# Optimization experiments

Hardware: AMD Instinct MI355X
Metric: run time of the kernel (lower is better)

Reference implementation:

```python
import jax, jax.numpy as jnp
import numpy as np

N_NODES = 2048
N_FLUID = 400000
N_SOLID = 400000


def setup_inputs() -> dict:
    key = jax.random.key(0)
    k1, k2, k3 = jax.random.split(key, 3)
    nodes = jax.random.uniform(k1, (N_NODES, 3), dtype=jnp.float32)
    # sorted distinct node ids per tet: sort 4 draws from [0, N-4) then add offsets 0..3
    fe = jnp.sort(jax.random.randint(k2, (N_FLUID, 4), 0, N_NODES - 4), axis=1) + jnp.arange(4)
    se = jnp.sort(jax.random.randint(k3, (N_SOLID, 4), 0, N_NODES - 4), axis=1) + jnp.arange(4)
    return {
        "nodes": nodes,
        "fluid_elements": fe.astype(jnp.int32),
        "solid_elements": se.astype(jnp.int32),
        "E_mod": jnp.float32(2.1e11),
        "nu": jnp.float32(0.3),
        "rho_s": jnp.float32(7850.0),
    }


def _grads_and_volume(coords):
    """coords: [E,4,3] -> shape-fn gradients [E,4,3], volume [E]."""
    ones = jnp.ones(coords.shape[:-1] + (1,), coords.dtype)
    A = jnp.concatenate([ones, coords], axis=-1)
    A_inv = jnp.linalg.inv(A)
    grads = jnp.swapaxes(A_inv[..., 1:, :], -1, -2)        # [E,4,3]
    v0 = coords[:, 1] - coords[:, 0]
    v1 = coords[:, 2] - coords[:, 0]
    v2 = coords[:, 3] - coords[:, 0]
    vol = jnp.abs(jnp.linalg.det(jnp.stack([v0, v1, v2], axis=-1))) / 6.0  # [E]
    return grads, vol


def _fluid_element_matrices(coords):
    grads, vol = _grads_and_volume(coords)
    K_e = vol[:, None, None] * jnp.einsum("eik,ejk->eij", grads, grads)      # [E,4,4]
    m_template = (2.0 * jnp.eye(4, dtype=coords.dtype) + jnp.ones((4, 4), coords.dtype)) / 10.0
    M_e = vol[:, None, None] * m_template
    return K_e, M_e


def _elasticity_D(E_mod, nu):
    coeff = E_mod / ((1.0 + nu) * (1.0 - 2.0 * nu))
    top = nu * jnp.ones((3, 3), jnp.float32) + (1.0 - 2.0 * nu) * jnp.eye(3, dtype=jnp.float32)
    D = jnp.zeros((6, 6), jnp.float32)
    D = D.at[:3, :3].set(top)
    D = D.at[3:, 3:].set(((1.0 - 2.0 * nu) / 2.0) * jnp.eye(3, dtype=jnp.float32))
    return coeff * D


def _solid_element_matrices(coords, E_mod, nu, rho_s):
    grads, vol = _grads_and_volume(coords)                 # grads [E,4,3]
    bx, by, bz = grads[..., 0], grads[..., 1], grads[..., 2]   # each [E,4]
    z = jnp.zeros_like(bx)
    # per-node 6x3 strain-displacement block -> [E,4,6,3]
    block = jnp.stack([
        jnp.stack([bx, z, z], axis=-1),
        jnp.stack([z, by, z], axis=-1),
        jnp.stack([z, z, bz], axis=-1),
        jnp.stack([by, bx, z], axis=-1),
        jnp.stack([z, bz, by], axis=-1),
        jnp.stack([bz, z, bx], axis=-1),
    ], axis=-2)
    E = coords.shape[0]
    B = jnp.transpose(block, (0, 2, 1, 3)).reshape(E, 6, 12)  # [E,6,12]
    D = _elasticity_D(E_mod, nu)                              # [6,6]
    K_e = vol[:, None, None] * jnp.einsum("eai,ab,ebj->eij", B, D, B)  # [E,12,12]
    M_e = (rho_s * vol / 4.0)[:, None, None] * jnp.eye(12, dtype=coords.dtype)
    return K_e, M_e


def reference(nodes, fluid_elements, solid_elements, E_mod, nu, rho_s):
    n = nodes.shape[0]
    # ---- fluid: local matrices + scatter-add assembly into [N,N] ----
    cf = nodes[fluid_elements]                              # [Ef,4,3]
    Kf_e, Mf_e = _fluid_element_matrices(cf)
    rows = fluid_elements[:, :, None]                       # [Ef,4,1]
    cols = fluid_elements[:, None, :]                       # [Ef,1,4]
    K_f = jnp.zeros((n, n), jnp.float32).at[rows, cols].add(Kf_e)
    M_f = jnp.zeros((n, n), jnp.float32).at[rows, cols].add(Mf_e)
    # ---- solid: 3 dof/node, assembly into [3N,3N] ----
    cs = nodes[solid_elements]                              # [Es,4,3]
    Ks_e, Ms_e = _solid_element_matrices(cs, E_mod, nu, rho_s)
    dofs = (3 * solid_elements[:, :, None] + jnp.arange(3)).reshape(solid_elements.shape[0], 12)
    K_s = jnp.zeros((3 * n, 3 * n), jnp.float32).at[dofs[:, :, None], dofs[:, None, :]].add(Ks_e)
    M_s = jnp.zeros((3 * n, 3 * n), jnp.float32).at[dofs[:, :, None], dofs[:, None, :]].add(Ms_e)
    return (K_f, M_f, K_s, M_s)
```

## Files before the change

### kernel.cpp

```cpp
#include <hip/hip_runtime.h>


#define G_PART 256

__device__ __forceinline__ float sel4(float x0, float x1, float x2, float x3, int a) {
    float r = x0;
    r = (a == 1) ? x1 : r;
    r = (a == 2) ? x2 : r;
    r = (a == 3) ? x3 : r;
    return r;
}
__device__ __forceinline__ int sel4i(int x0, int x1, int x2, int x3, int a) {
    int r = x0;
    r = (a == 1) ? x1 : r;
    r = (a == 2) ? x2 : r;
    r = (a == 3) ? x3 : r;
    return r;
}

__device__ __forceinline__ float wave_reduce(float v) {
#pragma unroll
    for (int m = 1; m < 64; m <<= 1) v += __shfl_xor(v, m, 64);
    return v;
}

__device__ __forceinline__ void tet_geom_f(const float* __restrict__ nodes,
                                           int n0, int n1, int n2, int n3_,
                                           float& gx1, float& gy1, float& gz1,
                                           float& gx2, float& gy2, float& gz2,
                                           float& gx3, float& gy3, float& gz3,
                                           float& volf)
{
    const float* q0 = nodes + 3ll * n0;
    const float* q1 = nodes + 3ll * n1;
    const float* q2 = nodes + 3ll * n2;
    const float* q3 = nodes + 3ll * n3_;
    double p0x = q0[0], p0y = q0[1], p0z = q0[2];
    double r1x = (double)q1[0] - p0x, r1y = (double)q1[1] - p0y, r1z = (double)q1[2] - p0z;
    double r2x = (double)q2[0] - p0x, r2y = (double)q2[1] - p0y, r2z = (double)q2[2] - p0z;
    double r3x = (double)q3[0] - p0x, r3y = (double)q3[1] - p0y, r3z = (double)q3[2] - p0z;
    double c23x = r2y*r3z - r2z*r3y, c23y = r2z*r3x - r2x*r3z, c23z = r2x*r3y - r2y*r3x;
    double det = r1x*c23x + r1y*c23y + r1z*c23z;
    double inv = 1.0 / det;
    double c31x = r3y*r1z - r3z*r1y, c31y = r3z*r1x - r3x*r1z, c31z = r3x*r1y - r3y*r1x;
    double c12x = r1y*r2z - r1z*r2y, c12y = r1z*r2x - r1x*r2z, c12z = r1x*r2y - r1y*r2x;
    gx1 = (float)(c23x*inv); gy1 = (float)(c23y*inv); gz1 = (float)(c23z*inv);
    gx2 = (float)(c31x*inv); gy2 = (float)(c31y*inv); gz2 = (float)(c31z*inv);
    gx3 = (float)(c12x*inv); gy3 = (float)(c12y*inv); gz3 = (float)(c12z*inv);
    volf = (float)(fabs(det) / 6.0);
}

__device__ __forceinline__ int fetch_entry(const int* __restrict__ ent,
                                           const int* __restrict__ Sb,
                                           const int* __restrict__ Qb,
                                           int chunk4, int v)
{
    int lo = 0, hi = 255;
#pragma unroll
    for (int it = 0; it < 8; ++it) {
        int mid = (lo + hi + 1) >> 1;
        bool ge = (Qb[mid] <= v);
        lo = ge ? mid : lo;
        hi = ge ? hi : mid - 1;
    }
    return ent[(size_t)lo * chunk4 + Sb[lo] + (v - Qb[lo])];
}

#define DECL_VISIT(P) \
    float P##gx0=0,P##gx1=0,P##gx2=0,P##gx3=0, P##gy0=0,P##gy1=0,P##gy2=0,P##gy3=0, \
          P##gz0=0,P##gz1=0,P##gz2=0,P##gz3=0, P##vol=0, P##ga0=0,P##ga1=0,P##ga2=0; \
    int P##a=0, P##c0=0,P##c1=0,P##c2=0,P##c3=0;

#define LOAD_VISIT(P, packed_) do { \
    int e_ = (packed_) >> 2; P##a = (packed_) & 3; \
    int4 nd_ = elems4[e_]; \
    P##c0 = nd_.x; P##c1 = nd_.y; P##c2 = nd_.z; P##c3 = nd_.w; \
    tet_geom_f(nodes, nd_.x, nd_.y, nd_.z, nd_.w, \
        P##gx1,P##gy1,P##gz1, P##gx2,P##gy2,P##gz2, P##gx3,P##gy3,P##gz3, P##vol); \
    P##gx0 = -(P##gx1+P##gx2+P##gx3); \
    P##gy0 = -(P##gy1+P##gy2+P##gy3); \
    P##gz0 = -(P##gz1+P##gz2+P##gz3); \
    P##ga0 = sel4(P##gx0,P##gx1,P##gx2,P##gx3,P##a); \
    P##ga1 = sel4(P##gy0,P##gy1,P##gy2,P##gy3,P##a); \
    P##ga2 = sel4(P##gz0,P##gz1,P##gz2,P##gz3,P##a); \
} while (0)

#define DIAG_S(P) do { \
    float lv_ = lam*P##vol, mv_ = mu*P##vol, lm_ = lv_+mv_; \
    float mgg_ = mv_*(P##ga0*P##ga0 + P##ga1*P##ga1 + P##ga2*P##ga2); \
    d00 += lm_*P##ga0*P##ga0 + mgg_; d01 += lm_*P##ga0*P##ga1;        d02 += lm_*P##ga0*P##ga2; \
    d10 += lm_*P##ga1*P##ga0;        d11 += lm_*P##ga1*P##ga1 + mgg_; d12 += lm_*P##ga1*P##ga2; \
    d20 += lm_*P##ga2*P##ga0;        d21 += lm_*P##ga2*P##ga1;        d22 += lm_*P##ga2*P##ga2 + mgg_; \
    vsum += P##vol; } while (0)

#define DIAG_F(P) do { \
    dK += P##vol*(P##ga0*P##ga0 + P##ga1*P##ga1 + P##ga2*P##ga2); \
    dM += P##vol*0.3f; } while (0)

#define PAIR_S(P, b_) do { \
    float gb0_ = sel4(P##gx0,P##gx1,P##gx2,P##gx3,b_); \
    float gb1_ = sel4(P##gy0,P##gy1,P##gy2,P##gy3,b_); \
    float gb2_ = sel4(P##gz0,P##gz1,P##gz2,P##gz3,b_); \
    col = sel4i(P##c0,P##c1,P##c2,P##c3,b_); \
    float lv_ = lam*P##vol, mv_ = mu*P##vol; \
    float la0_ = lv_*P##ga0, la1_ = lv_*P##ga1, la2_ = lv_*P##ga2; \
    float ma0_ = mv_*P##ga0, ma1_ = mv_*P##ga1, ma2_ = mv_*P##ga2; \
    float mgg_ = mv_*(P##ga0*gb0_ + P##ga1*gb1_ + P##ga2*gb2_); \
    v00 = la0_*gb0_ + ma0_*gb0_ + mgg_; v01 = la0_*gb1_ + ma1_*gb0_; v02 = la0_*gb2_ + ma2_*gb0_; \
    v10 = la1_*gb0_ + ma0_*gb1_; v11 = la1_*gb1_ + ma1_*gb1_ + mgg_; v12 = la1_*gb2_ + ma2_*gb1_; \
    v20 = la2_*gb0_ + ma0_*gb2_; v21 = la2_*gb1_ + ma1_*gb2_; v22 = la2_*gb2_ + ma2_*gb2_ + mgg_; \
} while (0)

#define PAIR_F(P, b_) do { \
    float gb0_ = sel4(P##gx0,P##gx1,P##gx2,P##gx3,b_); \
    float gb1_ = sel4(P##gy0,P##gy1,P##gy2,P##gy3,b_); \
    float gb2_ = sel4(P##gz0,P##gz1,P##gz2,P##gz3,b_); \
    col = sel4i(P##c0,P##c1,P##c2,P##c3,b_); \
    vK = P##vol*(P##ga0*gb0_ + P##ga1*gb1_ + P##ga2*gb2_); \
    vM = P##vol*0.1f; \
} while (0)

__global__ void __launch_bounds__(256)
index_build(const int4* __restrict__ fe, const int4* __restrict__ se,
            int* __restrict__ entF, int* __restrict__ entS,
            int* __restrict__ PF, int* __restrict__ PS,
            int nf, int ns, int n, int chunkF, int chunkS)
{
    extern __shared__ int h[];
    int* wsum = h + n;
    const bool solid = blockIdx.x >= G_PART;
    const int b = solid ? blockIdx.x - G_PART : blockIdx.x;
    const int4* elems = solid ? se : fe;
    const int nelem = solid ? ns : nf;
    const int chunk = solid ? chunkS : chunkF;
    int* P = (solid ? PS : PF) + (size_t)b * (n + 1);
    int* entries = (solid ? entS : entF) + (size_t)b * 4 * chunk;

    const int t = threadIdx.x;
    const int beg = b * chunk, end = min(nelem, beg + chunk);

    for (int i = t; i < n; i += 256) h[i] = 0;
    __syncthreads();
    for (int e = beg + t; e < end; e += 256) {
        int4 nd = elems[e];
        atomicAdd(&h[nd.x], 1);
        atomicAdd(&h[nd.y], 1);
        atomicAdd(&h[nd.z], 1);
        atomicAdd(&h[nd.w], 1);
    }
    __syncthreads();

    const int cs = (n + 255) / 256;
    const int base = t * cs;
    int s = 0;
    for (int k = 0; k < cs; ++k) {
        int i = base + k;
        if (i < n) s += h[i];
    }
    wsum[t] = s;
    __syncthreads();
    for (int d = 1; d < 256; d <<= 1) {
        int v = (t >= d) ? wsum[t - d] : 0;
        __syncthreads();
        wsum[t] += v;
        __syncthreads();
    }
    int run = (t == 0) ? 0 : wsum[t - 1];
    for (int k = 0; k < cs; ++k) {
        int i = base + k;
        if (i < n) { int c = h[i]; h[i] = run; P[i] = run; run += c; }
    }
    if (t == 255) P[n] = wsum[255];
    __syncthreads();

    for (int e = beg + t; e < end; e += 256) {
        int4 nd = elems[e];
        int p;
        p = atomicAdd(&h[nd.x], 1); entries[p] = e * 4 + 0;
        p = atomicAdd(&h[nd.y], 1); entries[p] = e * 4 + 1;
        p = atomicAdd(&h[nd.z], 1); entries[p] = e * 4 + 2;
        p = atomicAdd(&h[nd.w], 1); entries[p] = e * 4 + 3;
    }
}

__global__ void __launch_bounds__(512, 4)
fused_gather(const int* __restrict__ entF, const int* __restrict__ PF,
             const int* __restrict__ entS, const int* __restrict__ PS,
             const int4* __restrict__ fe, const int4* __restrict__ se,
             const float* __restrict__ nodes,
             float* __restrict__ Kf, float* __restrict__ Mf,
             float* __restrict__ Ks, float* __restrict__ Ms,
             const float* __restrict__ E_p, const float* __restrict__ nu_p,
             const float* __restrict__ rho_p, int n, int n3,
             int chunk4F, int chunk4S)
{
    extern __shared__ unsigned char smem[];
    const int tid = threadIdx.x;
    const int bid = blockIdx.x;

    if (bid < n) {
        const int r = bid;
        const int4* elems4 = se;
        float* val = (float*)smem;
        unsigned short* claim = (unsigned short*)(val + 9 * n);
        int* Sb = (int*)(claim + n);
        int* Qb = Sb + 256;
        float* dred = (float*)(Qb + 257);

        {
            float4* v = (float4*)val;
            int cnt = (9 * n) >> 2;
            for (int k = tid; k < cnt; k += 512) v[k] = make_float4(0.f,0.f,0.f,0.f);
        }
        if (tid < 256) {
            const int* Pp = PS + (size_t)tid * (n + 1) + r;
            int s0 = Pp[0], e0 = Pp[1];
            Sb[tid] = s0;
            Qb[tid] = e0 - s0;
        }
        __syncthreads();
        if (tid < 64) {
            int c0 = Qb[4*tid], c1 = Qb[4*tid+1], c2 = Qb[4*tid+2], c3 = Qb[4*tid+3];
            int s = c0 + c1 + c2 + c3;
            int x = s;
#pragma unroll
            for (int d = 1; d < 64; d <<= 1) {
                int y = __shfl_up(x, d, 64);
                if (tid >= d) x += y;
            }
            int ex = x - s;
            Qb[4*tid] = ex; Qb[4*tid+1] = ex + c0;
            Qb[4*tid+2] = ex + c0 + c1; Qb[4*tid+3] = ex + c0 + c1 + c2;
            if (tid == 63) Qb[256] = ex + s;
        }
        __syncthreads();
        const int T = Qb[256];

        float E = *E_p, nu = *nu_p, rho = *rho_p;
        float coeff = E / ((1.f + nu) * (1.f - 2.f * nu));
        float lam = coeff * nu;
        float mu  = coeff * (1.f - 2.f * nu) * 0.5f;

        float d00=0,d01=0,d02=0,d10=0,d11=0,d12=0,d20=0,d21=0,d22=0,vsum=0;
        DECL_VISIT(A_);
        DECL_VISIT(B_);

        bool pending = false, validB = false;
        int s, col = 0, nextV = tid + 1024;
        float v00=0,v01=0,v02=0,v10=0,v11=0,v12=0,v20=0,v21=0,v22=0;

        const int vi0 = tid, vi1 = tid + 512;
        if (vi0 < T) {
            int pk = fetch_entry(entS, Sb, Qb, chunk4S, vi0);
            LOAD_VISIT(A_, pk); DIAG_S(A_); s = 0;
        } else s = 6;
        if (vi1 < T) {
            int pk = fetch_entry(entS, Sb, Qb, chunk4S, vi1);
            LOAD_VISIT(B_, pk); DIAG_S(B_); validB = true;
        }

        auto advanceS = [&]() {
            while (!pending) {
                if (s >= 6 || (s >= 3 && !validB)) {
                    if (nextV >= T) return;
                    int pk = fetch_entry(entS, Sb, Qb, chunk4S, nextV);
                    LOAD_VISIT(B_, pk); DIAG_S(B_);
                    validB = true; nextV += 512; s = 3;
                }
                if (s < 3) { int t_ = s;     int b_ = t_ + (t_ >= A_a ? 1 : 0); PAIR_S(A_, b_); }
                else       { int t_ = s - 3; int b_ = t_ + (t_ >= B_a ? 1 : 0); PAIR_S(B_, b_); }
                ++s; pending = true;
            }
        };

        advanceS();
        int live = __syncthreads_count(pending ? 1 : 0);
        while (live) {
            if (pending) claim[col] = (unsigned short)tid;
            __syncthreads();
            if (pending && claim[col] == (unsigned short)tid) {
                float* p0 = val + 3 * col;
                float* p1 = p0 + n3;
                float* p2 = p1 + n3;
                p0[0]+=v00; p0[1]+=v01; p0[2]+=v02;
                p1[0]+=v10; p1[1]+=v11; p1[2]+=v12;
                p2[0]+=v20; p2[1]+=v21; p2[2]+=v22;
                pending = false;
                advanceS();
            }
            live = __syncthreads_count(pending ? 1 : 0);
        }

        d00=wave_reduce(d00); d01=wave_reduce(d01); d02=wave_reduce(d02);
        d10=wave_reduce(d10); d11=wave_reduce(d11); d12=wave_reduce(d12);
        d20=wave_reduce(d20); d21=wave_reduce(d21); d22=wave_reduce(d22);
        vsum=wave_reduce(vsum);
        if ((tid & 63) == 0) {
            int w = tid >> 6;
            dred[w*10+0]=d00; dred[w*10+1]=d01; dred[w*10+2]=d02;
            dred[w*10+3]=d10; dred[w*10+4]=d11; dred[w*10+5]=d12;
            dred[w*10+6]=d20; dred[w*10+7]=d21; dred[w*10+8]=d22;
            dred[w*10+9]=vsum;
        }
        __syncthreads();
        if (tid < 10) {
            float t_ = 0.f;
            for (int w = 0; w < 8; ++w) t_ += dred[w*10 + tid];
            dred[80 + tid] = t_;
        }
        __syncthreads();
        if (tid < 9) {
            int i = tid / 3, j = tid - 3 * i;
            val[i * n3 + 3 * r + j] += dred[80 + tid];
        }
        __syncthreads();

        int q = n3 >> 2;
        for (int k4 = tid; k4 < 3 * q; k4 += 512) {
            int i = (k4 >= q) + (k4 >= 2*q);
            int t4 = k4 - i * q;
            float4 w = ((const float4*)(val + i * n3))[t4];
            ((float4*)(Ks + (size_t)(3*r + i) * n3))[t4] = w;
        }
        float diag = rho * 0.25f * dred[89];
        for (int k4 = tid; k4 < 3 * q; k4 += 512) {
            int i = (k4 >= q) + (k4 >= 2*q);
            int t4 = k4 - i * q;
            int dcol = 3*r + i;
            int base = t4 << 2;
            float4 w;
            w.x = (base + 0 == dcol) ? diag : 0.f;
            w.y = (base + 1 == dcol) ? diag : 0.f;
            w.z = (base + 2 == dcol) ? diag : 0.f;
            w.w = (base + 3 == dcol) ? diag : 0.f;
            ((float4*)(Ms + (size_t)(3*r + i) * n3))[t4] = w;
        }
    } else {
        const int r = bid - n;
        const int4* elems4 = fe;
        float* val = (float*)smem;
        unsigned short* claim = (unsigned short*)(val + 2 * n);
        int* Sb = (int*)(claim + n);
        int* Qb = Sb + 256;
        float* dred = (float*)(Qb + 257);

        {
            float4* v = (float4*)val;
            int cnt = (2 * n) >> 2;
            for (int k = tid; k < cnt; k += 512) v[k] = make_float4(0.f,0.f,0.f,0.f);
        }
        if (tid < 256) {
            const int* Pp = PF + (size_t)tid * (n + 1) + r;
            int s0 = Pp[0], e0 = Pp[1];
            Sb[tid] = s0;
            Qb[tid] = e0 - s0;
        }
        __syncthreads();
        if (tid < 64) {
            int c0 = Qb[4*tid], c1 = Qb[4*tid+1], c2 = Qb[4*tid+2], c3 = Qb[4*tid+3];
            int s = c0 + c1 + c2 + c3;
            int x = s;
#pragma unroll
            for (int d = 1; d < 64; d <<= 1) {
                int y = __shfl_up(x, d, 64);
                if (tid >= d) x += y;
            }
            int ex = x - s;
            Qb[4*tid] = ex; Qb[4*tid+1] = ex + c0;
            Qb[4*tid+2] = ex + c0 + c1; Qb[4*tid+3] = ex + c0 + c1 + c2;
            if (tid == 63) Qb[256] = ex + s;
        }
        __syncthreads();
        const int T = Qb[256];

        float dK = 0.f, dM = 0.f;
        DECL_VISIT(A_);
        DECL_VISIT(B_);

        bool pending = false, validB = false;
        int s, col = 0, nextV = tid + 1024;
        float vK = 0.f, vM = 0.f;

        const int vi0 = tid, vi1 = tid + 512;
        if (vi0 < T) {
            int pk = fetch_entry(entF, Sb, Qb, chunk4F, vi0);
            LOAD_VISIT(A_, pk); DIAG_F(A_); s = 0;
        } else s = 6;
        if (vi1 < T) {
            int pk = fetch_entry(entF, Sb, Qb, chunk4F, vi1);
            LOAD_VISIT(B_, pk); DIAG_F(B_); validB = true;
        }

        auto advanceF = [&]() {
            while (!pending) {
                if (s >= 6 || (s >= 3 && !validB)) {
                    if (nextV >= T) return;
                    int pk = fetch_entry(entF, Sb, Qb, chunk4F, nextV);
                    LOAD_VISIT(B_, pk); DIAG_F(B_);
                    validB = true; nextV += 512; s = 3;
                }
                if (s < 3) { int t_ = s;     int b_ = t_ + (t_ >= A_a ? 1 : 0); PAIR_F(A_, b_); }
                else       { int t_ = s - 3; int b_ = t_ + (t_ >= B_a ? 1 : 0); PAIR_F(B_, b_); }
                ++s; pending = true;
            }
        };

        advanceF();
        int live = __syncthreads_count(pending ? 1 : 0);
        while (live) {
            if (pending) claim[col] = (unsigned short)tid;
            __syncthreads();
            if (pending && claim[col] == (unsigned short)tid) {
                val[col]     += vK;
                val[n + col] += vM;
                pending = false;
                advanceF();
            }
            live = __syncthreads_count(pending ? 1 : 0);
        }

        dK = wave_reduce(dK);
        dM = wave_reduce(dM);
        if ((tid & 63) == 0) { int w = tid >> 6; dred[w*2+0] = dK; dred[w*2+1] = dM; }
        __syncthreads();
        if (tid < 2) {
            float t_ = 0.f;
            for (int w = 0; w < 8; ++w) t_ += dred[w*2 + tid];
            dred[16 + tid] = t_;
        }
        __syncthreads();
        if (tid == 0) { val[r] += dred[16]; val[n + r] += dred[17]; }
        __syncthreads();

        size_t rowoff = (size_t)r * n;
        int qf = n >> 2;
        float4* K4 = (float4*)(Kf + rowoff);
        float4* M4 = (float4*)(Mf + rowoff);
        for (int c4 = tid; c4 < qf; c4 += 512) {
            K4[c4] = ((const float4*)val)[c4];
            M4[c4] = ((const float4*)(val + n))[c4];
        }
    }
}

__device__ __forceinline__ void tet_grads_d(const float* __restrict__ nodes,
                                            const int* ni, double g[4][3], double& vol)
{
    double p[4][3];
#pragma unroll
    for (int a = 0; a < 4; ++a) {
        const float* q = nodes + 3ll * ni[a];
        p[a][0] = (double)q[0]; p[a][1] = (double)q[1]; p[a][2] = (double)q[2];
    }
    double r1[3], r2[3], r3[3];
#pragma unroll
    for (int k = 0; k < 3; ++k) {
        r1[k] = p[1][k] - p[0][k];
        r2[k] = p[2][k] - p[0][k];
        r3[k] = p[3][k] - p[0][k];
    }
    double c23[3] = { r2[1]*r3[2]-r2[2]*r3[1], r2[2]*r3[0]-r2[0]*r3[2], r2[0]*r3[1]-r2[1]*r3[0] };
    double det = r1[0]*c23[0] + r1[1]*c23[1] + r1[2]*c23[2];
    double inv = 1.0 / det;
    double c31[3] = { r3[1]*r1[2]-r3[2]*r1[1], r3[2]*r1[0]-r3[0]*r1[2], r3[0]*r1[1]-r3[1]*r1[0] };
    double c12[3] = { r1[1]*r2[2]-r1[2]*r2[1], r1[2]*r2[0]-r1[0]*r2[2], r1[0]*r2[1]-r1[1]*r2[0] };
#pragma unroll
    for (int k = 0; k < 3; ++k) {
        g[1][k] = c23[k]*inv; g[2][k] = c31[k]*inv; g[3][k] = c12[k]*inv;
        g[0][k] = -(g[1][k] + g[2][k] + g[3][k]);
    }
    vol = fabs(det) / 6.0;
}

__global__ void __launch_bounds__(256)
fluid_assemble(const float* __restrict__ nodes, const int* __restrict__ elems,
               float* __restrict__ Kf, float* __restrict__ Mf, int nelem, int n)
{
    int e = blockIdx.x * blockDim.x + threadIdx.x;
    if (e >= nelem) return;
    const int4 nd = *reinterpret_cast<const int4*>(elems + 4ll * e);
    int ni[4] = { nd.x, nd.y, nd.z, nd.w };
    double g[4][3], vol;
    tet_grads_d(nodes, ni, g, vol);
#pragma unroll
    for (int a = 0; a < 4; ++a) {
        long long rowoff = (long long)ni[a] * n;
#pragma unroll
        for (int b = 0; b < 4; ++b) {
            double kv = vol * (g[a][0]*g[b][0] + g[a][1]*g[b][1] + g[a][2]*g[b][2]);
            double mv = vol * (a == b ? 0.3 : 0.1);
            atomicAdd(Kf + rowoff + ni[b], (float)kv);
            atomicAdd(Mf + rowoff + ni[b], (float)mv);
        }
    }
}

__global__ void __launch_bounds__(256)
solid_assemble(const float* __restrict__ nodes, const int* __restrict__ elems,
               float* __restrict__ Ks, float* __restrict__ Ms,
               const float* __restrict__ E_p, const float* __restrict__ nu_p,
               const float* __restrict__ rho_p, int nelem, int n3)
{
    int e = blockIdx.x * blockDim.x + threadIdx.x;
    if (e >= nelem) return;
    double E = (double)*E_p, nu = (double)*nu_p, rho = (double)*rho_p;
    double coeff = E / ((1.0 + nu) * (1.0 - 2.0 * nu));
    double lam = coeff * nu, mu = coeff * (1.0 - 2.0 * nu) * 0.5;
    const int4 nd = *reinterpret_cast<const int4*>(elems + 4ll * e);
    int ni[4] = { nd.x, nd.y, nd.z, nd.w };
    double g[4][3], vol;
    tet_grads_d(nodes, ni, g, vol);
    double lv = lam * vol, mv = mu * vol;
#pragma unroll
    for (int a = 0; a < 4; ++a) {
        long long row0 = 3ll * ni[a];
#pragma unroll
        for (int b = 0; b < 4; ++b) {
            long long col0 = 3ll * ni[b];
            double gg = g[a][0]*g[b][0] + g[a][1]*g[b][1] + g[a][2]*g[b][2];
#pragma unroll
            for (int i = 0; i < 3; ++i) {
                float* rowp = Ks + (row0 + i) * (long long)n3 + col0;
#pragma unroll
                for (int j = 0; j < 3; ++j) {
                    double val = lv * g[a][i] * g[b][j] + mv * g[a][j] * g[b][i];
                    if (i == j) val += mv * gg;
                    atomicAdd(rowp + j, (float)val);
                }
            }
        }
        float mval = (float)(rho * vol * 0.25);
#pragma unroll
        for (int i = 0; i < 3; ++i) {
            long long d = row0 + i;
            atomicAdd(Ms + d * (long long)n3 + d, mval);
        }
    }
}

extern "C" void kernel_launch(void* const* d_in, const int* in_sizes, int n_in,
                              void* d_out, int out_size, void* d_ws, size_t ws_size,
                              hipStream_t stream)
{
    const float* nodes = (const float*)d_in[0];
    const int*   fe    = (const int*)d_in[1];
    const int*   se    = (const int*)d_in[2];
    const float* E_p   = (const float*)d_in[3];
    const float* nu_p  = (const float*)d_in[4];
    const float* rho_p = (const float*)d_in[5];

    const int n  = in_sizes[0] / 3;
    const int nf = in_sizes[1] / 4;
    const int ns = in_sizes[2] / 4;
    const int n3 = 3 * n;

    float* out = (float*)d_out;
    float* Kf = out;
    float* Mf = Kf + (size_t)n * n;
    float* Ks = Mf + (size_t)n * n;
    float* Ms = Ks + (size_t)n3 * n3;

    const int chunkF = (nf + G_PART - 1) / G_PART;
    const int chunkS = (ns + G_PART - 1) / G_PART;

    size_t pos = 0;
    auto take = [&](size_t bytes) {
        size_t p = pos;
        pos = (pos + bytes + 255) & ~(size_t)255;
        return p;
    };
    size_t entF_o = take((size_t)4 * chunkF * G_PART * 4);
    size_t entS_o = take((size_t)4 * chunkS * G_PART * 4);
    size_t PF_o   = take((size_t)G_PART * (n + 1) * 4);
    size_t PS_o   = take((size_t)G_PART * (n + 1) * 4);

    size_t gatherLds = (size_t)9 * n * 4 + (size_t)n * 2 + (256 + 257) * 4 + 96 * 4;
    size_t indexLds  = (size_t)(n + 256) * 4;
    bool gather_ok = (pos <= ws_size) && ((n & 3) == 0) && (n <= 65535) &&
                     (gatherLds <= 160 * 1024) && (indexLds <= 64 * 1024);

    const int bs = 256;

    if (!gather_ok) {
        hipMemsetAsync(d_out, 0, (size_t)out_size * sizeof(float), stream);
        fluid_assemble<<<(nf + bs - 1) / bs, bs, 0, stream>>>(nodes, fe, Kf, Mf, nf, n);
        solid_assemble<<<(ns + bs - 1) / bs, bs, 0, stream>>>(nodes, se, Ks, Ms,
                                                              E_p, nu_p, rho_p, ns, n3);
        return;
    }

    char* ws = (char*)d_ws;
    int* entF = (int*)(ws + entF_o);
    int* entS = (int*)(ws + entS_o);
    int* PF   = (int*)(ws + PF_o);
    int* PS   = (int*)(ws + PS_o);

    const int4* fe4 = (const int4*)fe;
    const int4* se4 = (const int4*)se;

    index_build<<<2 * G_PART, bs, indexLds, stream>>>(fe4, se4, entF, entS, PF, PS,
                                                      nf, ns, n, chunkF, chunkS);
    fused_gather<<<2 * n, 512, gatherLds, stream>>>(entF, PF, entS, PS,
                                                    fe4, se4, nodes,
                                                    Kf, Mf, Ks, Ms,
                                                    E_p, nu_p, rho_p, n, n3,
                                                    4 * chunkF, 4 * chunkS);
}
```

Baseline: 199.6 us.

## Use 1024-thread gather blocks with transposed prefix layout and claim-based visit lookup

Doubles the gather block size so each thread handles one visit instead of two, simplifying the per-thread state machine. The per-partition prefix arrays are stored node-major so a row's 256 partition offsets are read contiguously. The first visit's partition is found through an LDS claim map filled before the loop, avoiding the binary search. This adds an extra LDS fill pass and barrier and tightens the LDS budget check, which risks occupancy and synchronisation cost with larger blocks.

```diff
diff --git a/kernel.cpp b/kernel.cpp
--- a/kernel.cpp
+++ b/kernel.cpp
@@ -2,6 +2,8 @@
 
 
 #define G_PART 256
+#define GT 1024
+#define GW (GT / 64)
 
 __device__ __forceinline__ float sel4(float x0, float x1, float x2, float x3, int a) {
     float r = x0;
@@ -50,10 +52,10 @@
     volf = (float)(fabs(det) / 6.0);
 }
 
-__device__ __forceinline__ int fetch_entry(const int* __restrict__ ent,
-                                           const int* __restrict__ Sb,
-                                           const int* __restrict__ Qb,
-                                           int chunk4, int v)
+__device__ __forceinline__ int fetch_entry_bs(const int* __restrict__ ent,
+                                              const int* __restrict__ Sb,
+                                              const int* __restrict__ Qb,
+                                              int chunk4, int v)
 {
     int lo = 0, hi = 255;
 #pragma unroll
@@ -66,58 +68,58 @@
     return ent[(size_t)lo * chunk4 + Sb[lo] + (v - Qb[lo])];
 }
 
-#define DECL_VISIT(P) \
-    float P##gx0=0,P##gx1=0,P##gx2=0,P##gx3=0, P##gy0=0,P##gy1=0,P##gy2=0,P##gy3=0, \
-          P##gz0=0,P##gz1=0,P##gz2=0,P##gz3=0, P##vol=0, P##ga0=0,P##ga1=0,P##ga2=0; \
-    int P##a=0, P##c0=0,P##c1=0,P##c2=0,P##c3=0;
-
-#define LOAD_VISIT(P, packed_) do { \
-    int e_ = (packed_) >> 2; P##a = (packed_) & 3; \
+#define DECL_VISIT() \
+    float gxx0=0,gxx1=0,gxx2=0,gxx3=0, gyy0=0,gyy1=0,gyy2=0,gyy3=0, \
+          gzz0=0,gzz1=0,gzz2=0,gzz3=0, volv=0, ga0=0,ga1=0,ga2=0; \
+    int va=0, vc0=0,vc1=0,vc2=0,vc3=0;
+
+#define LOAD_VISIT(packed_) do { \
+    int e_ = (packed_) >> 2; va = (packed_) & 3; \
     int4 nd_ = elems4[e_]; \
-    P##c0 = nd_.x; P##c1 = nd_.y; P##c2 = nd_.z; P##c3 = nd_.w; \
-    tet_geom_f(nodes, nd_.x, nd_.y, nd_.z, nd_.w, \
-        P##gx1,P##gy1,P##gz1, P##gx2,P##gy2,P##gz2, P##gx3,P##gy3,P##gz3, P##vol); \
-    P##gx0 = -(P##gx1+P##gx2+P##gx3); \
-    P##gy0 = -(P##gy1+P##gy2+P##gy3); \
-    P##gz0 = -(P##gz1+P##gz2+P##gz3); \
-    P##ga0 = sel4(P##gx0,P##gx1,P##gx2,P##gx3,P##a); \
-    P##ga1 = sel4(P##gy0,P##gy1,P##gy2,P##gy3,P##a); \
-    P##ga2 = sel4(P##gz0,P##gz1,P##gz2,P##gz3,P##a); \
+    vc0 = nd_.x; vc1 = nd_.y; vc2 = nd_.z; vc3 = nd_.w; \
+    tet_geom_f(nodes, vc0, vc1, vc2, vc3, \
+        gxx1,gyy1,gzz1, gxx2,gyy2,gzz2, gxx3,gyy3,gzz3, volv); \
+    gxx0 = -(gxx1+gxx2+gxx3); \
+    gyy0 = -(gyy1+gyy2+gyy3); \
+    gzz0 = -(gzz1+gzz2+gzz3); \
+    ga0 = sel4(gxx0,gxx1,gxx2,gxx3,va); \
+    ga1 = sel4(gyy0,gyy1,gyy2,gyy3,va); \
+    ga2 = sel4(gzz0,gzz1,gzz2,gzz3,va); \
 } while (0)
 
-#define DIAG_S(P) do { \
-    float lv_ = lam*P##vol, mv_ = mu*P##vol, lm_ = lv_+mv_; \
-    float mgg_ = mv_*(P##ga0*P##ga0 + P##ga1*P##ga1 + P##ga2*P##ga2); \
-    d00 += lm_*P##ga0*P##ga0 + mgg_; d01 += lm_*P##ga0*P##ga1;        d02 += lm_*P##ga0*P##ga2; \
-    d10 += lm_*P##ga1*P##ga0;        d11 += lm_*P##ga1*P##ga1 + mgg_; d12 += lm_*P##ga1*P##ga2; \
-    d20 += lm_*P##ga2*P##ga0;        d21 += lm_*P##ga2*P##ga1;        d22 += lm_*P##ga2*P##ga2 + mgg_; \
-    vsum += P##vol; } while (0)
-
-#define DIAG_F(P) do { \
-    dK += P##vol*(P##ga0*P##ga0 + P##ga1*P##ga1 + P##ga2*P##ga2); \
-    dM += P##vol*0.3f; } while (0)
-
-#define PAIR_S(P, b_) do { \
-    float gb0_ = sel4(P##gx0,P##gx1,P##gx2,P##gx3,b_); \
-    float gb1_ = sel4(P##gy0,P##gy1,P##gy2,P##gy3,b_); \
-    float gb2_ = sel4(P##gz0,P##gz1,P##gz2,P##gz3,b_); \
-    col = sel4i(P##c0,P##c1,P##c2,P##c3,b_); \
-    float lv_ = lam*P##vol, mv_ = mu*P##vol; \
-    float la0_ = lv_*P##ga0, la1_ = lv_*P##ga1, la2_ = lv_*P##ga2; \
-    float ma0_ = mv_*P##ga0, ma1_ = mv_*P##ga1, ma2_ = mv_*P##ga2; \
-    float mgg_ = mv_*(P##ga0*gb0_ + P##ga1*gb1_ + P##ga2*gb2_); \
+#define DIAG_S() do { \
+    float lv_ = lam*volv, mv_ = mu*volv, lm_ = lv_+mv_; \
+    float mgg_ = mv_*(ga0*ga0 + ga1*ga1 + ga2*ga2); \
+    d00 += lm_*ga0*ga0 + mgg_; d01 += lm_*ga0*ga1;        d02 += lm_*ga0*ga2; \
+    d10 += lm_*ga1*ga0;        d11 += lm_*ga1*ga1 + mgg_; d12 += lm_*ga1*ga2; \
+    d20 += lm_*ga2*ga0;        d21 += lm_*ga2*ga1;        d22 += lm_*ga2*ga2 + mgg_; \
+    vsum += volv; } while (0)
+
+#define DIAG_F() do { \
+    dK += volv*(ga0*ga0 + ga1*ga1 + ga2*ga2); \
+    dM += volv*0.3f; } while (0)
+
+#define PAIR_S(b_) do { \
+    float gb0_ = sel4(gxx0,gxx1,gxx2,gxx3,b_); \
+    float gb1_ = sel4(gyy0,gyy1,gyy2,gyy3,b_); \
+    float gb2_ = sel4(gzz0,gzz1,gzz2,gzz3,b_); \
+    col = sel4i(vc0,vc1,vc2,vc3,b_); \
+    float lv_ = lam*volv, mv_ = mu*volv; \
+    float la0_ = lv_*ga0, la1_ = lv_*ga1, la2_ = lv_*ga2; \
+    float ma0_ = mv_*ga0, ma1_ = mv_*ga1, ma2_ = mv_*ga2; \
+    float mgg_ = mv_*(ga0*gb0_ + ga1*gb1_ + ga2*gb2_); \
     v00 = la0_*gb0_ + ma0_*gb0_ + mgg_; v01 = la0_*gb1_ + ma1_*gb0_; v02 = la0_*gb2_ + ma2_*gb0_; \
     v10 = la1_*gb0_ + ma0_*gb1_; v11 = la1_*gb1_ + ma1_*gb1_ + mgg_; v12 = la1_*gb2_ + ma2_*gb1_; \
     v20 = la2_*gb0_ + ma0_*gb2_; v21 = la2_*gb1_ + ma1_*gb2_; v22 = la2_*gb2_ + ma2_*gb2_ + mgg_; \
 } while (0)
 
-#define PAIR_F(P, b_) do { \
-    float gb0_ = sel4(P##gx0,P##gx1,P##gx2,P##gx3,b_); \
-    float gb1_ = sel4(P##gy0,P##gy1,P##gy2,P##gy3,b_); \
-    float gb2_ = sel4(P##gz0,P##gz1,P##gz2,P##gz3,b_); \
-    col = sel4i(P##c0,P##c1,P##c2,P##c3,b_); \
-    vK = P##vol*(P##ga0*gb0_ + P##ga1*gb1_ + P##ga2*gb2_); \
-    vM = P##vol*0.1f; \
+#define PAIR_F(b_) do { \
+    float gb0_ = sel4(gxx0,gxx1,gxx2,gxx3,b_); \
+    float gb1_ = sel4(gyy0,gyy1,gyy2,gyy3,b_); \
+    float gb2_ = sel4(gzz0,gzz1,gzz2,gzz3,b_); \
+    col = sel4i(vc0,vc1,vc2,vc3,b_); \
+    vK = volv*(ga0*gb0_ + ga1*gb1_ + ga2*gb2_); \
+    vM = volv*0.1f; \
 } while (0)
 
 __global__ void __launch_bounds__(256)
@@ -133,7 +135,7 @@
     const int4* elems = solid ? se : fe;
     const int nelem = solid ? ns : nf;
     const int chunk = solid ? chunkS : chunkF;
-    int* P = (solid ? PS : PF) + (size_t)b * (n + 1);
+    int* P2 = solid ? PS : PF;
     int* entries = (solid ? entS : entF) + (size_t)b * 4 * chunk;
 
     const int t = threadIdx.x;
@@ -168,9 +170,13 @@
     int run = (t == 0) ? 0 : wsum[t - 1];
     for (int k = 0; k < cs; ++k) {
         int i = base + k;
-        if (i < n) { int c = h[i]; h[i] = run; P[i] = run; run += c; }
-    }
-    if (t == 255) P[n] = wsum[255];
+        if (i < n) {
+            int c = h[i]; h[i] = run;
+            P2[(size_t)i * G_PART + b] = run;
+            run += c;
+        }
+    }
+    if (t == 255) P2[(size_t)n * G_PART + b] = wsum[255];
     __syncthreads();
 
     for (int e = beg + t; e < end; e += 256) {
@@ -183,7 +189,7 @@
     }
 }
 
-__global__ void __launch_bounds__(512, 4)
+__global__ void __launch_bounds__(GT, 2)
 fused_gather(const int* __restrict__ entF, const int* __restrict__ PF,
              const int* __restrict__ entS, const int* __restrict__ PS,
              const int4* __restrict__ fe, const int4* __restrict__ se,
@@ -210,11 +216,11 @@
         {
             float4* v = (float4*)val;
             int cnt = (9 * n) >> 2;
-            for (int k = tid; k < cnt; k += 512) v[k] = make_float4(0.f,0.f,0.f,0.f);
+            for (int k = tid; k < cnt; k += GT) v[k] = make_float4(0.f,0.f,0.f,0.f);
         }
         if (tid < 256) {
-            const int* Pp = PS + (size_t)tid * (n + 1) + r;
-            int s0 = Pp[0], e0 = Pp[1];
+            int s0 = PS[(size_t)r * G_PART + tid];
+            int e0 = PS[(size_t)(r + 1) * G_PART + tid];
             Sb[tid] = s0;
             Qb[tid] = e0 - s0;
         }
@@ -235,6 +241,13 @@
         }
         __syncthreads();
         const int T = Qb[256];
+        const int pvLim = min(T, n);
+
+        if (tid < 256) {
+            int v0 = Qb[tid], v1 = min(Qb[tid + 1], pvLim);
+            for (int v = v0; v < v1; ++v) claim[v] = (unsigned short)tid;
+        }
+        __syncthreads();
 
         float E = *E_p, nu = *nu_p, rho = *rho_p;
         float coeff = E / ((1.f + nu) * (1.f - 2.f * nu));
@@ -242,38 +255,38 @@
         float mu  = coeff * (1.f - 2.f * nu) * 0.5f;
 
         float d00=0,d01=0,d02=0,d10=0,d11=0,d12=0,d20=0,d21=0,d22=0,vsum=0;
-        DECL_VISIT(A_);
-        DECL_VISIT(B_);
-
-        bool pending = false, validB = false;
-        int s, col = 0, nextV = tid + 1024;
+        DECL_VISIT();
+
+        bool pending = false;
+        int s = 3, col = 0, nextV = tid + GT;
         float v00=0,v01=0,v02=0,v10=0,v11=0,v12=0,v20=0,v21=0,v22=0;
 
-        const int vi0 = tid, vi1 = tid + 512;
-        if (vi0 < T) {
-            int pk = fetch_entry(entS, Sb, Qb, chunk4S, vi0);
-            LOAD_VISIT(A_, pk); DIAG_S(A_); s = 0;
-        } else s = 6;
-        if (vi1 < T) {
-            int pk = fetch_entry(entS, Sb, Qb, chunk4S, vi1);
-            LOAD_VISIT(B_, pk); DIAG_S(B_); validB = true;
+        if (tid < T) {
+            int part = (tid < pvLim) ? (int)claim[tid]
+                                     : 0;
+            int pk = (tid < pvLim)
+                   ? entS[(size_t)part * chunk4S + Sb[part] + (tid - Qb[part])]
+                   : fetch_entry_bs(entS, Sb, Qb, chunk4S, tid);
+            LOAD_VISIT(pk); DIAG_S(); s = 0;
         }
 
         auto advanceS = [&]() {
             while (!pending) {
-                if (s >= 6 || (s >= 3 && !validB)) {
+                if (s >= 3) {
                     if (nextV >= T) return;
-                    int pk = fetch_entry(entS, Sb, Qb, chunk4S, nextV);
-                    LOAD_VISIT(B_, pk); DIAG_S(B_);
-                    validB = true; nextV += 512; s = 3;
+                    int pk = fetch_entry_bs(entS, Sb, Qb, chunk4S, nextV);
+                    LOAD_VISIT(pk); DIAG_S();
+                    s = 0; nextV += GT;
                 }
-                if (s < 3) { int t_ = s;     int b_ = t_ + (t_ >= A_a ? 1 : 0); PAIR_S(A_, b_); }
-                else       { int t_ = s - 3; int b_ = t_ + (t_ >= B_a ? 1 : 0); PAIR_S(B_, b_); }
+                int b_ = s + ((s >= va) ? 1 : 0);
+                PAIR_S(b_);
                 ++s; pending = true;
             }
         };
 
         advanceS();
+        __syncthreads();
+
         int live = __syncthreads_count(pending ? 1 : 0);
         while (live) {
             if (pending) claim[col] = (unsigned short)tid;
@@ -305,25 +318,25 @@
         __syncthreads();
         if (tid < 10) {
             float t_ = 0.f;
-            for (int w = 0; w < 8; ++w) t_ += dred[w*10 + tid];
-            dred[80 + tid] = t_;
+            for (int w = 0; w < GW; ++w) t_ += dred[w*10 + tid];
+            dred[GW*10 + tid] = t_;
         }
         __syncthreads();
         if (tid < 9) {
             int i = tid / 3, j = tid - 3 * i;
-            val[i * n3 + 3 * r + j] += dred[80 + tid];
+            val[i * n3 + 3 * r + j] += dred[GW*10 + tid];
         }
         __syncthreads();
 
         int q = n3 >> 2;
-        for (int k4 = tid; k4 < 3 * q; k4 += 512) {
+        for (int k4 = tid; k4 < 3 * q; k4 += GT) {
             int i = (k4 >= q) + (k4 >= 2*q);
             int t4 = k4 - i * q;
             float4 w = ((const float4*)(val + i * n3))[t4];
             ((float4*)(Ks + (size_t)(3*r + i) * n3))[t4] = w;
         }
-        float diag = rho * 0.25f * dred[89];
-        for (int k4 = tid; k4 < 3 * q; k4 += 512) {
+        float diag = rho * 0.25f * dred[GW*10 + 9];
+        for (int k4 = tid; k4 < 3 * q; k4 += GT) {
             int i = (k4 >= q) + (k4 >= 2*q);
             int t4 = k4 - i * q;
             int dcol = 3*r + i;
@@ -347,11 +360,11 @@
         {
             float4* v = (float4*)val;
             int cnt = (2 * n) >> 2;
-            for (int k = tid; k < cnt; k += 512) v[k] = make_float4(0.f,0.f,0.f,0.f);
+            for (int k = tid; k < cnt; k += GT) v[k] = make_float4(0.f,0.f,0.f,0.f);
         }
         if (tid < 256) {
-            const int* Pp = PF + (size_t)tid * (n + 1) + r;
-            int s0 = Pp[0], e0 = Pp[1];
+            int s0 = PF[(size_t)r * G_PART + tid];
+            int e0 = PF[(size_t)(r + 1) * G_PART + tid];
             Sb[tid] = s0;
             Qb[tid] = e0 - s0;
         }
@@ -372,40 +385,46 @@
         }
         __syncthreads();
         const int T = Qb[256];
+        const int pvLim = min(T, n);
+
+        if (tid < 256) {
+            int v0 = Qb[tid], v1 = min(Qb[tid + 1], pvLim);
+            for (int v = v0; v < v1; ++v) claim[v] = (unsigned short)tid;
+        }
+        __syncthreads();
 
         float dK = 0.f, dM = 0.f;
-        DECL_VISIT(A_);
-        DECL_VISIT(B_);
-
-        bool pending = false, validB = false;
-        int s, col = 0, nextV = tid + 1024;
+        DECL_VISIT();
+
+        bool pending = false;
+        int s = 3, col = 0, nextV = tid + GT;
         float vK = 0.f, vM = 0.f;
 
-        const int vi0 = tid, vi1 = tid + 512;
-        if (vi0 < T) {
-            int pk = fetch_entry(entF, Sb, Qb, chunk4F, vi0);
-            LOAD_VISIT(A_, pk); DIAG_F(A_); s = 0;
-        } else s = 6;
-        if (vi1 < T) {
-            int pk = fetch_entry(entF, Sb, Qb, chunk4F, vi1);
-            LOAD_VISIT(B_, pk); DIAG_F(B_); validB = true;
+        if (tid < T) {
+            int part = (tid < pvLim) ? (int)claim[tid] : 0;
+            int pk = (tid < pvLim)
+                   ? entF[(size_t)part * chunk4F + Sb[part] + (tid - Qb[part])]
+                   : fetch_entry_bs(entF, Sb, Qb, chunk4F, tid);
+            LOAD_VISIT(pk); DIAG_F(); s = 0;
         }
 
         auto advanceF = [&]() {
             while (!pending) {
-                if (s >= 6 || (s >= 3 && !validB)) {
+                if (s >= 3) {
                     if (nextV >= T) return;
-                    int pk = fetch_entry(entF, Sb, Qb, chunk4F, nextV);
-                    LOAD_VISIT(B_, pk); DIAG_F(B_);
-                    validB = true; nextV += 512; s = 3;
+                    int pk = fetch_entry_bs(entF, Sb, Qb, chunk4F, nextV);
+                    LOAD_VISIT(pk); DIAG_F();
+                    s = 0; nextV += GT;
                 }
-                if (s < 3) { int t_ = s;     int b_ = t_ + (t_ >= A_a ? 1 : 0); PAIR_F(A_, b_); }
-                else       { int t_ = s - 3; int b_ = t_ + (t_ >= B_a ? 1 : 0); PAIR_F(B_, b_); }
+                int b_ = s + ((s >= va) ? 1 : 0);
+                PAIR_F(b_);
                 ++s; pending = true;
             }
         };
 
         advanceF();
+        __syncthreads();
+
         int live = __syncthreads_count(pending ? 1 : 0);
         while (live) {
             if (pending) claim[col] = (unsigned short)tid;
@@ -425,18 +444,18 @@
         __syncthreads();
         if (tid < 2) {
             float t_ = 0.f;
-            for (int w = 0; w < 8; ++w) t_ += dred[w*2 + tid];
-            dred[16 + tid] = t_;
-        }
-        __syncthreads();
-        if (tid == 0) { val[r] += dred[16]; val[n + r] += dred[17]; }
+            for (int w = 0; w < GW; ++w) t_ += dred[w*2 + tid];
+            dred[GW*2 + tid] = t_;
+        }
+        __syncthreads();
+        if (tid == 0) { val[r] += dred[GW*2]; val[n + r] += dred[GW*2 + 1]; }
         __syncthreads();
 
         size_t rowoff = (size_t)r * n;
         int qf = n >> 2;
         float4* K4 = (float4*)(Kf + rowoff);
         float4* M4 = (float4*)(Mf + rowoff);
-        for (int c4 = tid; c4 < qf; c4 += 512) {
+        for (int c4 = tid; c4 < qf; c4 += GT) {
             K4[c4] = ((const float4*)val)[c4];
             M4[c4] = ((const float4*)(val + n))[c4];
         }
@@ -571,13 +590,14 @@
     };
     size_t entF_o = take((size_t)4 * chunkF * G_PART * 4);
     size_t entS_o = take((size_t)4 * chunkS * G_PART * 4);
-    size_t PF_o   = take((size_t)G_PART * (n + 1) * 4);
-    size_t PS_o   = take((size_t)G_PART * (n + 1) * 4);
-
-    size_t gatherLds = (size_t)9 * n * 4 + (size_t)n * 2 + (256 + 257) * 4 + 96 * 4;
+    size_t PF_o   = take((size_t)(n + 1) * G_PART * 4);
+    size_t PS_o   = take((size_t)(n + 1) * G_PART * 4);
+
+    size_t gatherLds = (size_t)9 * n * 4 + (size_t)n * 2 + (256 + 257) * 4
+                     + (GW * 10 + 10) * 4;
     size_t indexLds  = (size_t)(n + 256) * 4;
     bool gather_ok = (pos <= ws_size) && ((n & 3) == 0) && (n <= 65535) &&
-                     (gatherLds <= 160 * 1024) && (indexLds <= 64 * 1024);
+                     (gatherLds <= 80 * 1024) && (indexLds <= 64 * 1024);
 
     const int bs = 256;
 
@@ -600,9 +620,9 @@
 
     index_build<<<2 * G_PART, bs, indexLds, stream>>>(fe4, se4, entF, entS, PF, PS,
                                                       nf, ns, n, chunkF, chunkS);
-    fused_gather<<<2 * n, 512, gatherLds, stream>>>(entF, PF, entS, PS,
-                                                    fe4, se4, nodes,
-                                                    Kf, Mf, Ks, Ms,
-                                                    E_p, nu_p, rho_p, n, n3,
-                                                    4 * chunkF, 4 * chunkS);
-}
+    fused_gather<<<2 * n, GT, gatherLds, stream>>>(entF, PF, entS, PS,
+                                                   fe4, se4, nodes,
+                                                   Kf, Mf, Ks, Ms,
+                                                   E_p, nu_p, rho_p, n, n3,
+                                                   4 * chunkF, 4 * chunkS);
+}
```

Measured after the change: 294.2 us. +47.4%, slower.
